# Performance work log

Measured on AMD Instinct MI355X. Metric: run time of the kernel, lower is better.

The kernel has to match this reference:

```python
import jax, jax.numpy as jnp
import numpy as np

HID = 128
HEADS = 4
CH = HID // HEADS          # 32
EDGE_DIM = 2 * HID         # H_update mode
GROUPS = 8
NEG_SLOPE = 0.2
EPS_GN = 1e-5
EPS_LN = 1e-5
N_NODES = 32768
N_EDGES = 524288


def setup_inputs() -> dict:
    key = jax.random.key(0)
    ks = jax.random.split(key, 32)
    N, E, C = N_NODES, N_EDGES, HID
    s = lambda fan: 1.0 / np.sqrt(fan)
    inp = dict(
        h_target=jax.random.normal(ks[0], (N, C), jnp.float32),
        h_source=jax.random.normal(ks[1], (N, C), jnp.float32),
        pos=jax.random.normal(ks[2], (N, 2), jnp.float32),
        t_emb=jax.random.normal(ks[3], (N, C), jnp.float32),
        edge_index=jax.random.randint(ks[4], (2, E), 0, N, jnp.int32),
        # AdaGN params
        gn_gamma=jnp.ones((C,), jnp.float32),
        gn_beta=jnp.zeros((C,), jnp.float32),
        fc_W=jax.random.normal(ks[5], (C, 2 * C), jnp.float32) * s(C),
        fc_b=jnp.zeros((2 * C,), jnp.float32),
        # GATv2 params
        Wl=jax.random.normal(ks[6], (C, HEADS * CH), jnp.float32) * s(C),
        bl=jnp.zeros((HEADS * CH,), jnp.float32),
        Wr=jax.random.normal(ks[7], (C, HEADS * CH), jnp.float32) * s(C),
        br=jnp.zeros((HEADS * CH,), jnp.float32),
        We=jax.random.normal(ks[8], (EDGE_DIM, HEADS * CH), jnp.float32) * s(EDGE_DIM),
        att=jax.random.normal(ks[9], (HEADS, CH), jnp.float32) * s(CH),
        gat_bias=jnp.zeros((HEADS * CH,), jnp.float32),
        # post GAT linear
        Wpost=jax.random.normal(ks[10], (C, C), jnp.float32) * s(C),
        bpost=jnp.zeros((C,), jnp.float32),
        # update MLP: LayerNorm -> Linear -> GELU -> Linear
        ln_g=jnp.ones((C,), jnp.float32),
        ln_b=jnp.zeros((C,), jnp.float32),
        W1=jax.random.normal(ks[11], (C, C), jnp.float32) * s(C),
        b1=jnp.zeros((C,), jnp.float32),
        W2=jax.random.normal(ks[12], (C, C), jnp.float32) * s(C),
        b2=jnp.zeros((C,), jnp.float32),
    )
    return inp


def _adagn(x, cond, gn_gamma, gn_beta, fc_W, fc_b):
    N, C = x.shape
    xg = x.reshape(N, GROUPS, C // GROUPS)
    mu = xg.mean(-1, keepdims=True)
    var = xg.var(-1, keepdims=True)
    normed = ((xg - mu) * jax.lax.rsqrt(var + EPS_GN)).reshape(N, C)
    normed = normed * gn_gamma + gn_beta
    style = cond @ fc_W + fc_b
    gamma, beta = jnp.split(style, 2, axis=-1)
    return normed * (1.0 + gamma) + beta


def reference(h_target, h_source, pos, t_emb, edge_index,
              gn_gamma, gn_beta, fc_W, fc_b,
              Wl, bl, Wr, br, We, att, gat_bias,
              Wpost, bpost, ln_g, ln_b, W1, b1, W2, b2):
    N, C = h_source.shape
    src, dst = edge_index[0], edge_index[1]

    h_src_mod = _adagn(h_source, t_emb, gn_gamma, gn_beta, fc_W, fc_b)

    # physics edge features (H_update mode)
    d_vec = pos[src] - pos[dst]                       # [E,2]
    dx, dy = d_vec[:, 0:1], d_vec[:, 1:2]
    dist_sq = jnp.maximum((d_vec ** 2).sum(-1, keepdims=True), 1e-8)
    grad_mag = (h_src_mod[src] - h_src_mod[dst]) / dist_sq   # [E,C]
    edge_attr = jnp.concatenate([grad_mag * (-dy), grad_mag * dx], axis=-1)  # [E,2C]

    # GATv2Conv (eval mode, no dropout)
    xl = (h_src_mod @ Wl + bl).reshape(N, HEADS, CH)  # source transform
    xr = (h_src_mod @ Wr + br).reshape(N, HEADS, CH)  # target transform
    e = (edge_attr @ We).reshape(-1, HEADS, CH)
    z = jax.nn.leaky_relu(xl[src] + xr[dst] + e, NEG_SLOPE)   # [E,H,Ch]
    logit = jnp.einsum('ehc,hc->eh', z, att)                  # [E,H]
    m = jax.ops.segment_max(logit, dst, num_segments=N)       # [N,H]
    m = jnp.where(jnp.isfinite(m), m, 0.0)
    ex = jnp.exp(logit - m[dst])
    denom = jax.ops.segment_sum(ex, dst, num_segments=N)      # [N,H]
    alpha = ex / (denom[dst] + 1e-16)                         # [E,H]
    msg = xl[src] * alpha[..., None]                          # [E,H,Ch]
    aggr = jax.ops.segment_sum(msg, dst, num_segments=N).reshape(N, HEADS * CH)
    aggr = aggr + gat_bias

    aggr = aggr @ Wpost + bpost

    # update MLP with residual
    mu = aggr.mean(-1, keepdims=True)
    var = aggr.var(-1, keepdims=True)
    ln = (aggr - mu) * jax.lax.rsqrt(var + EPS_LN) * ln_g + ln_b
    h = jax.nn.gelu(ln @ W1 + b1, approximate=False) @ W2 + b2
    return h_target + h
```

## Files before the change

### kernel.cpp

```cpp
#include <hip/hip_runtime.h>
#include <hip/hip_bf16.h>
#include <math.h>

#define HID 128

typedef __bf16 bf16x8 __attribute__((ext_vector_type(8)));
typedef float f32x4 __attribute__((ext_vector_type(4)));
typedef float nf4 __attribute__((ext_vector_type(4)));
union BF8 { uint4 u; bf16x8 v; unsigned short s[8]; };
struct U3 { unsigned x, y, z; };

__device__ __forceinline__ unsigned short f2bf(float x) {
  unsigned u = __float_as_uint(x);
  unsigned r = u + 0x7FFFu + ((u >> 16) & 1u);
  return (unsigned short)(r >> 16);
}
__device__ __forceinline__ float bf2f(unsigned short h) {
  return __uint_as_float(((unsigned)h) << 16);
}
__device__ __forceinline__ void ld2bf(const unsigned short* p, float& x, float& y) {
  unsigned v = *(const unsigned*)p;
  x = __uint_as_float((v & 0xFFFFu) << 16);
  y = __uint_as_float(v & 0xFFFF0000u);
}
__device__ __forceinline__ float2 unpk(unsigned w) {
  return make_float2(__uint_as_float(w << 16), __uint_as_float(w & 0xFFFF0000u));
}
__device__ __forceinline__ float2 pk_add2(float2 a, float2 b) {
  return make_float2(a.x + b.x, a.y + b.y);
}
__device__ __forceinline__ float2 pk_sub2(float2 a, float2 b) {
  return make_float2(a.x - b.x, a.y - b.y);
}
__device__ __forceinline__ float2 pk_fma2(float2 a, float2 b, float2 c) {
  return make_float2(fmaf(a.x, b.x, c.x), fmaf(a.y, b.y, c.y));
}
__device__ __forceinline__ float2 pk_max2(float2 a, float2 b) {
  return make_float2(fmaxf(a.x, b.x), fmaxf(a.y, b.y));
}
__device__ __forceinline__ float2 pk_muls2(float2 a, float b) {
  return make_float2(a.x * b, a.y * b);
}

__global__ __launch_bounds__(256) void k1_prep_zero(
    const float* __restrict__ fc_W, const float* __restrict__ Wl,
    const float* __restrict__ Wr, const float* __restrict__ We,
    const float* __restrict__ Wpost, const float* __restrict__ W1,
    const float* __restrict__ W2, const float* __restrict__ bl,
    const float* __restrict__ br, const float* __restrict__ gat_bias,
    const float* __restrict__ bpost,
    unsigned short* __restrict__ fcTh, unsigned short* __restrict__ fcTl,
    unsigned short* __restrict__ WnTh, unsigned short* __restrict__ WnTl,
    unsigned short* __restrict__ WpT, unsigned short* __restrict__ W1T,
    unsigned short* __restrict__ W2T,
    float* __restrict__ bxy, float* __restrict__ bpost2,
    int* __restrict__ count) {
  int bid = blockIdx.x;
  if (bid >= 578) {
    int i = (bid - 578) * 256 + threadIdx.x;
    ((int4*)count)[i] = make_int4(0, 0, 0, 0);
    return;
  }
  int gid = bid * 256 + threadIdx.x;
  if (gid < 32768) {
    int n = gid >> 7, k = gid & 127;
    float x = fc_W[k * 256 + n];
    unsigned short h = f2bf(x);
    fcTh[n * 128 + k] = h;
    fcTl[n * 128 + k] = f2bf(x - bf2f(h));
  } else if (gid < 98304) {
    int i = gid - 32768; int n = i >> 7, k = i & 127;
    float x;
    if (n < 128)      x = Wl[k * 128 + n];
    else if (n < 256) x = Wr[k * 128 + (n - 128)];
    else if (n < 384) x = We[k * 128 + (n - 256)];
    else              x = We[(128 + k) * 128 + (n - 384)];
    unsigned short h = f2bf(x);
    WnTh[n * 128 + k] = h;
    if (n >= 256) WnTl[(n - 256) * 128 + k] = f2bf(x - bf2f(h));
  } else if (gid < 147456) {
    int i = gid - 98304; int which = i >> 14; int j = i & 16383;
    int n = j >> 7, k = j & 127;
    const float* W = (which == 0) ? Wpost : (which == 1) ? W1 : W2;
    unsigned short* T = (which == 0) ? WpT : (which == 1) ? W1T : W2T;
    T[n * 128 + k] = f2bf(W[k * 128 + n]);
  } else if (gid < 147712) {
    int j = gid - 147456;
    bxy[j] = (j < 128) ? bl[j] : br[j - 128];
  } else if (gid < 147840) {
    int t = gid - 147712;
    float s = bpost[t];
    for (int k = 0; k < 128; ++k) s += gat_bias[k] * Wpost[k * 128 + t];
    bpost2[t] = s;
  }
}

__global__ __launch_bounds__(256) void k2_style_hist(
    const float* __restrict__ A, const unsigned short* __restrict__ WTh,
    const unsigned short* __restrict__ WTl, const float* __restrict__ bias,
    float* __restrict__ C,
    const int* __restrict__ edst, int* __restrict__ count, int E) {
  if (blockIdx.x >= 512) {
    int e = (blockIdx.x - 512) * 256 + threadIdx.x;
    if (e < E) atomicAdd(&count[edst[e]], 1);
    return;
  }
  int tid = threadIdx.x;
  int wave = tid >> 6, lane = tid & 63;
  int m = lane & 15, q = lane >> 4;
  int r0 = blockIdx.x * 64 + wave * 16;
  const float* arow = A + (size_t)(r0 + m) * 128 + q * 8;
  BF8 Ah[4], Al[4];
#pragma unroll
  for (int kc = 0; kc < 4; ++kc) {
    float4 x0 = *(const float4*)(arow + kc * 32);
    float4 x1 = *(const float4*)(arow + kc * 32 + 4);
    float xs[8] = {x0.x, x0.y, x0.z, x0.w, x1.x, x1.y, x1.z, x1.w};
#pragma unroll
    for (int j = 0; j < 8; ++j) {
      unsigned short h = f2bf(xs[j]);
      Ah[kc].s[j] = h;
      Al[kc].s[j] = f2bf(xs[j] - bf2f(h));
    }
  }
  for (int nt = 0; nt < 16; ++nt) {
    const unsigned short* wr  = WTh + (size_t)(nt * 16 + m) * 128 + q * 8;
    const unsigned short* wrl = WTl + (size_t)(nt * 16 + m) * 128 + q * 8;
    f32x4 acc = {0.f, 0.f, 0.f, 0.f};
#pragma unroll
    for (int kc = 0; kc < 4; ++kc) {
      BF8 bh, blo;
      bh.u  = *(const uint4*)(wr + kc * 32);
      blo.u = *(const uint4*)(wrl + kc * 32);
      acc = __builtin_amdgcn_mfma_f32_16x16x32_bf16(Ah[kc].v, bh.v, acc, 0, 0, 0);
      acc = __builtin_amdgcn_mfma_f32_16x16x32_bf16(Al[kc].v, bh.v, acc, 0, 0, 0);
      acc = __builtin_amdgcn_mfma_f32_16x16x32_bf16(Ah[kc].v, blo.v, acc, 0, 0, 0);
    }
    int n = nt * 16 + m;
    float bv = bias[n];
#pragma unroll
    for (int i = 0; i < 4; ++i) {
      int row = r0 + q * 4 + i;
      C[(size_t)row * 256 + n] = acc[i] + bv;
    }
  }
}

__global__ __launch_bounds__(256) void k3_node_scan(
    const float* __restrict__ h_source, const float* __restrict__ style,
    const float* __restrict__ gn_gamma, const float* __restrict__ gn_beta,
    const unsigned short* __restrict__ WnTh, const unsigned short* __restrict__ WnTl,
    const float* __restrict__ bxy,
    unsigned short* __restrict__ packed, unsigned short* __restrict__ xrArr,
    const int* __restrict__ count, int* __restrict__ rowptr,
    int* __restrict__ cursor, int N, int E) {
  if (blockIdx.x == 256) {
    __shared__ int wtot[4];
    int t = threadIdx.x, lane = t & 63, wv = t >> 6;
    const int4* c4 = (const int4*)count;
    int base = t * 32;
    int s = 0;
    for (int i = 0; i < 32; ++i) {
      int4 c = c4[base + i];
      s += c.x + c.y + c.z + c.w;
    }
    int incl = s;
#pragma unroll
    for (int off = 1; off < 64; off <<= 1) {
      int v = __shfl_up(incl, off);
      if (lane >= off) incl += v;
    }
    if (lane == 63) wtot[wv] = incl;
    __syncthreads();
    if (t == 0) {
      int a0 = wtot[0], a1 = wtot[1], a2 = wtot[2];
      wtot[0] = 0; wtot[1] = a0; wtot[2] = a0 + a1; wtot[3] = a0 + a1 + a2;
    }
    __syncthreads();
    int run = wtot[wv] + incl - s;
    for (int i = 0; i < 32; ++i) {
      int4 c = c4[base + i];
      int4 r;
      r.x = run; run += c.x;
      r.y = run; run += c.y;
      r.z = run; run += c.z;
      r.w = run; run += c.w;
      ((int4*)rowptr)[base + i] = r;
      ((int4*)cursor)[base + i] = r;
    }
    if (t == 255) rowptr[N] = E;
    return;
  }
  int tid = threadIdx.x, wave = tid >> 6, lane = tid & 63;
  int m = lane & 15, q = lane >> 4;
  int r0 = blockIdx.x * 128 + wave * 32;
  BF8 Ah[2][4], Al[2][4];
#pragma unroll
  for (int set = 0; set < 2; ++set) {
    int r = r0 + set * 16 + m;
    const float* hrow = h_source + (size_t)r * 128;
    const float* srow = style + (size_t)r * 256;
#pragma unroll
    for (int kc = 0; kc < 4; ++kc) {
      int ch = q * 8 + kc * 32;
      float4 x0 = *(const float4*)(hrow + ch);
      float4 x1 = *(const float4*)(hrow + ch + 4);
      float xs[8] = {x0.x, x0.y, x0.z, x0.w, x1.x, x1.y, x1.z, x1.w};
      float s8 = 0.f, q8 = 0.f;
#pragma unroll
      for (int j = 0; j < 8; ++j) { s8 += xs[j]; q8 += xs[j] * xs[j]; }
      float s16 = s8 + __shfl_xor(s8, 16);
      float q16 = q8 + __shfl_xor(q8, 16);
      float mu = s16 * (1.0f / 16.0f);
      float var = q16 * (1.0f / 16.0f) - mu * mu;
      float rv = rsqrtf(var + 1e-5f);
      float4 g0 = *(const float4*)(gn_gamma + ch);
      float4 g1 = *(const float4*)(gn_gamma + ch + 4);
      float4 be0 = *(const float4*)(gn_beta + ch);
      float4 be1 = *(const float4*)(gn_beta + ch + 4);
      float4 sg0 = *(const float4*)(srow + ch);
      float4 sg1 = *(const float4*)(srow + ch + 4);
      float4 sb0 = *(const float4*)(srow + 128 + ch);
      float4 sb1 = *(const float4*)(srow + 128 + ch + 4);
      float gg[8] = {g0.x, g0.y, g0.z, g0.w, g1.x, g1.y, g1.z, g1.w};
      float bb[8] = {be0.x, be0.y, be0.z, be0.w, be1.x, be1.y, be1.z, be1.w};
      float sg[8] = {sg0.x, sg0.y, sg0.z, sg0.w, sg1.x, sg1.y, sg1.z, sg1.w};
      float sb[8] = {sb0.x, sb0.y, sb0.z, sb0.w, sb1.x, sb1.y, sb1.z, sb1.w};
#pragma unroll
      for (int j = 0; j < 8; ++j) {
        float v = ((xs[j] - mu) * rv * gg[j] + bb[j]) * (1.0f + sg[j]) + sb[j];
        unsigned short h = f2bf(v);
        Ah[set][kc].s[j] = h;
        Al[set][kc].s[j] = f2bf(v - bf2f(h));
      }
    }
  }
  for (int nt = 0; nt < 32; ++nt) {
    f32x4 acc0 = {0.f, 0.f, 0.f, 0.f};
    f32x4 acc1 = {0.f, 0.f, 0.f, 0.f};
    const unsigned short* wr = WnTh + (size_t)(nt * 16 + m) * 128 + q * 8;
    if (nt < 16) {
#pragma unroll
      for (int kc = 0; kc < 4; ++kc) {
        BF8 bh; bh.u = *(const uint4*)(wr + kc * 32);
        acc0 = __builtin_amdgcn_mfma_f32_16x16x32_bf16(Ah[0][kc].v, bh.v, acc0, 0, 0, 0);
        acc1 = __builtin_amdgcn_mfma_f32_16x16x32_bf16(Ah[1][kc].v, bh.v, acc1, 0, 0, 0);
      }
    } else {
      const unsigned short* wl = WnTl + (size_t)((nt - 16) * 16 + m) * 128 + q * 8;
#pragma unroll
      for (int kc = 0; kc < 4; ++kc) {
        BF8 bh, blo;
        bh.u  = *(const uint4*)(wr + kc * 32);
        blo.u = *(const uint4*)(wl + kc * 32);
        acc0 = __builtin_amdgcn_mfma_f32_16x16x32_bf16(Ah[0][kc].v, bh.v, acc0, 0, 0, 0);
        acc0 = __builtin_amdgcn_mfma_f32_16x16x32_bf16(Al[0][kc].v, bh.v, acc0, 0, 0, 0);
        acc0 = __builtin_amdgcn_mfma_f32_16x16x32_bf16(Ah[0][kc].v, blo.v, acc0, 0, 0, 0);
        acc1 = __builtin_amdgcn_mfma_f32_16x16x32_bf16(Ah[1][kc].v, bh.v, acc1, 0, 0, 0);
        acc1 = __builtin_amdgcn_mfma_f32_16x16x32_bf16(Al[1][kc].v, bh.v, acc1, 0, 0, 0);
        acc1 = __builtin_amdgcn_mfma_f32_16x16x32_bf16(Ah[1][kc].v, blo.v, acc1, 0, 0, 0);
      }
    }
    int n = nt * 16 + m;
    float bv = (nt < 16) ? bxy[n] : 0.0f;
#pragma unroll
    for (int set = 0; set < 2; ++set) {
      f32x4 a = set ? acc1 : acc0;
#pragma unroll
      for (int i = 0; i < 4; ++i) {
        int row = r0 + set * 16 + q * 4 + i;
        unsigned short h = f2bf(a[i] + bv);
        size_t pb = (size_t)row * 384;
        if (nt < 8)       packed[pb + (n >> 1) * 6 + (n & 1)] = h;
        else if (nt < 16) xrArr[(size_t)row * 128 + (n - 128)] = h;
        else if (nt < 24) { int c = n - 256; packed[pb + (c >> 1) * 6 + 2 + (c & 1)] = h; }
        else              { int c = n - 384; packed[pb + (c >> 1) * 6 + 4 + (c & 1)] = h; }
      }
    }
  }
}

__global__ __launch_bounds__(256) void k_scatter(const int* __restrict__ esrc,
                                                 const int* __restrict__ edst,
                                                 const float* __restrict__ pos,
                                                 int* __restrict__ cursor,
                                                 nf4* __restrict__ meta, int E) {
  int e = blockIdx.x * 256 + threadIdx.x;
  if (e >= E) return;
  int src = esrc[e], dst = edst[e];
  int p = atomicAdd(&cursor[dst], 1);
  float2 ps = *(const float2*)(pos + 2 * src);
  float2 pd = *(const float2*)(pos + 2 * dst);
  float dx = ps.x - pd.x, dy = ps.y - pd.y;
  float d2 = fmaxf(dx * dx + dy * dy, 1e-8f);
  nf4 v = {__int_as_float(src), -dy / d2, dx / d2, 0.0f};
  meta[p] = v;
}

__device__ __forceinline__ void edge_step(nf4 mt, const U3* __restrict__ packed3,
                                          int lane, float2 xr, float2 Ad, float2 Bd,
                                          float a0, float a1,
                                          float& m, float& l, float2& s) {
  int si = __float_as_int(mt.x);
  U3 w = packed3[(size_t)si * 64 + lane];
  float2 xl = unpk(w.x);
  float2 A  = unpk(w.y);
  float2 B  = unpk(w.z);
  float2 z = pk_add2(xl, xr);
  z = pk_fma2(make_float2(mt.y, mt.y), pk_sub2(A, Ad), z);
  z = pk_fma2(make_float2(mt.z, mt.z), pk_sub2(B, Bd), z);
  float2 zl = pk_max2(z, pk_muls2(z, 0.2f));
  float p = fmaf(a0, zl.x, a1 * zl.y);
#pragma unroll
  for (int mm = 8; mm >= 1; mm >>= 1) p += __shfl_xor(p, mm);
  if (p <= m) {
    float ex = __expf(p - m);
    l += ex;
    s = pk_fma2(make_float2(ex, ex), xl, s);
  } else {
    float sc = __expf(m - p);
    l = fmaf(l, sc, 1.0f);
    s = pk_fma2(make_float2(sc, sc), s, xl);
    m = p;
  }
}

__global__ __launch_bounds__(256) void k_edge(const int* __restrict__ rowptr,
                                              const nf4* __restrict__ meta,
                                              const unsigned short* __restrict__ packed,
                                              const unsigned short* __restrict__ xrArr,
                                              const float* __restrict__ att,
                                              unsigned* __restrict__ aggr16, int N) {
  int tid = threadIdx.x;
  int d = blockIdx.x * 4 + (tid >> 6);
  if (d >= N) return;
  int lane = tid & 63;
  int c0 = lane * 2;
  float2 av = *(const float2*)(att + c0);
  const U3* packed3 = (const U3*)packed;
  float2 xr, Ad, Bd;
  ld2bf(xrArr + (size_t)d * 128 + c0, xr.x, xr.y);
  {
    U3 wd = packed3[(size_t)d * 64 + lane];
    Ad = unpk(wd.y);
    Bd = unpk(wd.z);
  }
  int beg = rowptr[d], end = rowptr[d + 1];
  float m1 = -INFINITY, l1 = 0.f; float2 s1 = make_float2(0.f, 0.f);
  float m2 = -INFINITY, l2 = 0.f; float2 s2 = make_float2(0.f, 0.f);
  int j = beg;
  if (j + 1 < end) {
    nf4 mt0 = meta[j], mt1 = meta[j + 1];
    for (; j + 3 < end; j += 2) {
      nf4 nx0 = meta[j + 2], nx1 = meta[j + 3];
      edge_step(mt0, packed3, lane, xr, Ad, Bd, av.x, av.y, m1, l1, s1);
      edge_step(mt1, packed3, lane, xr, Ad, Bd, av.x, av.y, m2, l2, s2);
      mt0 = nx0; mt1 = nx1;
    }
    edge_step(mt0, packed3, lane, xr, Ad, Bd, av.x, av.y, m1, l1, s1);
    edge_step(mt1, packed3, lane, xr, Ad, Bd, av.x, av.y, m2, l2, s2);
    j += 2;
  }
  if (j < end) {
    nf4 mt = meta[j];
    edge_step(mt, packed3, lane, xr, Ad, Bd, av.x, av.y, m1, l1, s1);
  }
  float nm = fmaxf(m1, m2);
  float sc1 = (m1 == nm) ? 1.0f : __expf(m1 - nm);
  float sc2 = (m2 == nm) ? 1.0f : __expf(m2 - nm);
  float l = fmaf(l1, sc1, l2 * sc2);
  float o0 = fmaf(s1.x, sc1, s2.x * sc2);
  float o1 = fmaf(s1.y, sc1, s2.y * sc2);
  float inv = 1.0f / (l + 1e-16f);
  aggr16[(size_t)d * 64 + lane] = (unsigned)f2bf(o0 * inv) | ((unsigned)f2bf(o1 * inv) << 16);
}

__global__ __launch_bounds__(256) void k_mlp(const unsigned short* __restrict__ aggr16,
                                             const unsigned short* __restrict__ WpT,
                                             const unsigned short* __restrict__ W1T,
                                             const unsigned short* __restrict__ W2T,
                                             const float* __restrict__ bpost2,
                                             const float* __restrict__ b1,
                                             const float* __restrict__ b2,
                                             const float* __restrict__ ln_g,
                                             const float* __restrict__ ln_b,
                                             const float* __restrict__ h_target,
                                             float* __restrict__ out) {
  __shared__ unsigned short Tb[64 * 136];
  __shared__ unsigned short Ub[64 * 136];
  int tid = threadIdx.x, wave = tid >> 6, lane = tid & 63;
  int m = lane & 15, q = lane >> 4;
  int r0 = blockIdx.x * 64 + wave * 16;
  int rb0 = wave * 16;
  BF8 Af[4];
  {
    const unsigned short* arow = aggr16 + (size_t)(r0 + m) * 128 + q * 8;
#pragma unroll
    for (int kc = 0; kc < 4; ++kc) Af[kc].u = *(const uint4*)(arow + kc * 32);
  }
  f32x4 acc[8];
#pragma unroll
  for (int t = 0; t < 8; ++t) {
    const unsigned short* wr = WpT + (size_t)(t * 16 + m) * 128 + q * 8;
    f32x4 a = {0.f, 0.f, 0.f, 0.f};
#pragma unroll
    for (int kc = 0; kc < 4; ++kc) {
      BF8 bh; bh.u = *(const uint4*)(wr + kc * 32);
      a = __builtin_amdgcn_mfma_f32_16x16x32_bf16(Af[kc].v, bh.v, a, 0, 0, 0);
    }
    acc[t] = a;
  }
  float sum[4] = {0, 0, 0, 0}, sq[4] = {0, 0, 0, 0};
#pragma unroll
  for (int t = 0; t < 8; ++t) {
    float bv = bpost2[t * 16 + m];
#pragma unroll
    for (int i = 0; i < 4; ++i) {
      float v = acc[t][i] + bv;
      acc[t][i] = v;
      sum[i] += v;
      sq[i] += v * v;
    }
  }
#pragma unroll
  for (int i = 0; i < 4; ++i) {
#pragma unroll
    for (int w = 1; w <= 8; w <<= 1) {
      sum[i] += __shfl_xor(sum[i], w);
      sq[i] += __shfl_xor(sq[i], w);
    }
  }
  float mu[4], rv[4];
#pragma unroll
  for (int i = 0; i < 4; ++i) {
    mu[i] = sum[i] * (1.0f / 128.0f);
    float var = sq[i] * (1.0f / 128.0f) - mu[i] * mu[i];
    rv[i] = rsqrtf(var + 1e-5f);
  }
#pragma unroll
  for (int t = 0; t < 8; ++t) {
    int n = t * 16 + m;
    float g = ln_g[n], b = ln_b[n];
#pragma unroll
    for (int i = 0; i < 4; ++i) {
      float v = (acc[t][i] - mu[i]) * rv[i] * g + b;
      Tb[(rb0 + q * 4 + i) * 136 + n] = f2bf(v);
    }
  }
  __syncthreads();
  BF8 Bf[4];
  {
    const unsigned short* tp = Tb + (rb0 + m) * 136 + q * 8;
#pragma unroll
    for (int kc = 0; kc < 4; ++kc) Bf[kc].u = *(const uint4*)(tp + kc * 32);
  }
#pragma unroll
  for (int t = 0; t < 8; ++t) {
    const unsigned short* wr = W1T + (size_t)(t * 16 + m) * 128 + q * 8;
    f32x4 a = {0.f, 0.f, 0.f, 0.f};
#pragma unroll
    for (int kc = 0; kc < 4; ++kc) {
      BF8 bh; bh.u = *(const uint4*)(wr + kc * 32);
      a = __builtin_amdgcn_mfma_f32_16x16x32_bf16(Bf[kc].v, bh.v, a, 0, 0, 0);
    }
    acc[t] = a;
  }
#pragma unroll
  for (int t = 0; t < 8; ++t) {
    int n = t * 16 + m;
    float bv = b1[n];
#pragma unroll
    for (int i = 0; i < 4; ++i) {
      float v = acc[t][i] + bv;
      v = 0.5f * v * (1.0f + erff(v * 0.70710678118654752f));
      Ub[(rb0 + q * 4 + i) * 136 + n] = f2bf(v);
    }
  }
  __syncthreads();
  BF8 Cf[4];
  {
    const unsigned short* up = Ub + (rb0 + m) * 136 + q * 8;
#pragma unroll
    for (int kc = 0; kc < 4; ++kc) Cf[kc].u = *(const uint4*)(up + kc * 32);
  }
#pragma unroll
  for (int t = 0; t < 8; ++t) {
    const unsigned short* wr = W2T + (size_t)(t * 16 + m) * 128 + q * 8;
    f32x4 a = {0.f, 0.f, 0.f, 0.f};
#pragma unroll
    for (int kc = 0; kc < 4; ++kc) {
      BF8 bh; bh.u = *(const uint4*)(wr + kc * 32);
      a = __builtin_amdgcn_mfma_f32_16x16x32_bf16(Cf[kc].v, bh.v, a, 0, 0, 0);
    }
    int n = t * 16 + m;
    float bv = b2[n];
#pragma unroll
    for (int i = 0; i < 4; ++i) {
      size_t off = (size_t)(r0 + q * 4 + i) * 128 + n;
      out[off] = a[i] + bv + h_target[off];
    }
  }
}

extern "C" void kernel_launch(void* const* d_in, const int* in_sizes, int n_in,
                              void* d_out, int out_size, void* d_ws, size_t ws_size,
                              hipStream_t stream) {
  const float* h_target = (const float*)d_in[0];
  const float* h_source = (const float*)d_in[1];
  const float* pos      = (const float*)d_in[2];
  const float* t_emb    = (const float*)d_in[3];
  const int*   eidx     = (const int*)d_in[4];
  const float* gn_gamma = (const float*)d_in[5];
  const float* gn_beta  = (const float*)d_in[6];
  const float* fc_W     = (const float*)d_in[7];
  const float* fc_b     = (const float*)d_in[8];
  const float* Wl       = (const float*)d_in[9];
  const float* bl       = (const float*)d_in[10];
  const float* Wr       = (const float*)d_in[11];
  const float* br       = (const float*)d_in[12];
  const float* We       = (const float*)d_in[13];
  const float* att      = (const float*)d_in[14];
  const float* gat_bias = (const float*)d_in[15];
  const float* Wpost    = (const float*)d_in[16];
  const float* bpost    = (const float*)d_in[17];
  const float* ln_g     = (const float*)d_in[18];
  const float* ln_b     = (const float*)d_in[19];
  const float* W1       = (const float*)d_in[20];
  const float* b1       = (const float*)d_in[21];
  const float* W2       = (const float*)d_in[22];
  const float* b2       = (const float*)d_in[23];

  const int N = in_sizes[0] / HID;
  const int E = in_sizes[4] / 2;
  const int* esrc = eidx;
  const int* edst = eidx + E;

  float* ws = (float*)d_ws;
  const size_t MF = 1024 * 1024;
  float* style  = ws;
  unsigned* aggr16 = (unsigned*)ws;
  unsigned short* packed = (unsigned short*)(ws + 8 * MF);
  unsigned short* xrArr  = (unsigned short*)(ws + 14 * MF);
  nf4*   meta   = (nf4*)(ws + 16 * MF);
  int*   rowptr = (int*)(ws + 18 * MF);
  int*   count  = rowptr + 32832;
  int*   cursor = count + 32832;
  unsigned short* wgt = (unsigned short*)(ws + 18 * MF + 131072);
  unsigned short* fcTh = wgt;
  unsigned short* fcTl = wgt + 32768;
  unsigned short* WnTh = wgt + 65536;
  unsigned short* WnTl = wgt + 131072;
  unsigned short* WpT  = wgt + 163840;
  unsigned short* W1T  = wgt + 180224;
  unsigned short* W2T  = wgt + 196608;
  float* bxy    = (float*)(wgt + 212992);
  float* bpost2 = bxy + 256;
  const size_t needed = (size_t)(18 * MF + 131072 + 106496 + 512) * 4;
  if (ws_size < needed) return;

  dim3 blk(256);
  const int histB = (E + 255) / 256;

  k1_prep_zero<<<610, blk, 0, stream>>>(
      fc_W, Wl, Wr, We, Wpost, W1, W2, bl, br, gat_bias, bpost,
      fcTh, fcTl, WnTh, WnTl, WpT, W1T, W2T, bxy, bpost2, count);
  k2_style_hist<<<512 + histB, blk, 0, stream>>>(t_emb, fcTh, fcTl, fc_b, style,
                                                 edst, count, E);
  k3_node_scan<<<257, blk, 0, stream>>>(h_source, style, gn_gamma, gn_beta, WnTh, WnTl,
                                        bxy, packed, xrArr, count, rowptr, cursor, N, E);
  k_scatter<<<histB, blk, 0, stream>>>(esrc, edst, pos, cursor, meta, E);
  k_edge<<<(N + 3) / 4, blk, 0, stream>>>(rowptr, meta, packed, xrArr, att, aggr16, N);
  k_mlp<<<N / 64, blk, 0, stream>>>((const unsigned short*)aggr16, WpT, W1T, W2T, bpost2,
                                    b1, b2, ln_g, ln_b, h_target, (float*)d_out);
}
```

Baseline: 364.1 us.

## Stage MFMA outputs through swizzled LDS for coalesced global stores

The three GEMM kernels (style projection, node transform, final MLP) now write their MFMA accumulator fragments into per-wave shared memory, using XOR swizzles or padding, and then store full rows to global memory with wide coalesced writes. Before, each lane wrote scattered scalar floats or bf16 values. The node kernel now processes its two row sets one after another so the LDS tile fits, and the xr array is written and read as packed 32-bit words. The cost is large LDS allocations (64KB in k2 and k3), which limit occupancy, and the node kernel loses the weight-load reuse it had from interleaving the two sets.

```diff
diff --git a/kernel.cpp b/kernel.cpp
--- a/kernel.cpp
+++ b/kernel.cpp
@@ -17,11 +17,6 @@
 }
 __device__ __forceinline__ float bf2f(unsigned short h) {
   return __uint_as_float(((unsigned)h) << 16);
-}
-__device__ __forceinline__ void ld2bf(const unsigned short* p, float& x, float& y) {
-  unsigned v = *(const unsigned*)p;
-  x = __uint_as_float((v & 0xFFFFu) << 16);
-  y = __uint_as_float(v & 0xFFFF0000u);
 }
 __device__ __forceinline__ float2 unpk(unsigned w) {
   return make_float2(__uint_as_float(w << 16), __uint_as_float(w & 0xFFFF0000u));
@@ -100,6 +95,7 @@
     const unsigned short* __restrict__ WTl, const float* __restrict__ bias,
     float* __restrict__ C,
     const int* __restrict__ edst, int* __restrict__ count, int E) {
+  __shared__ float Lsf[16384];
   if (blockIdx.x >= 512) {
     int e = (blockIdx.x - 512) * 256 + threadIdx.x;
     if (e < E) atomicAdd(&count[edst[e]], 1);
@@ -109,6 +105,7 @@
   int wave = tid >> 6, lane = tid & 63;
   int m = lane & 15, q = lane >> 4;
   int r0 = blockIdx.x * 64 + wave * 16;
+  int wbase = wave * 4096;
   const float* arow = A + (size_t)(r0 + m) * 128 + q * 8;
   BF8 Ah[4], Al[4];
 #pragma unroll
@@ -140,9 +137,14 @@
     float bv = bias[n];
 #pragma unroll
     for (int i = 0; i < 4; ++i) {
-      int row = r0 + q * 4 + i;
-      C[(size_t)row * 256 + n] = acc[i] + bv;
-    }
+      int rl = q * 4 + i;
+      Lsf[wbase + rl * 256 + (n ^ (4 * (rl & 7)))] = acc[i] + bv;
+    }
+  }
+  for (int r = 0; r < 16; ++r) {
+    int cc = (4 * lane) ^ (4 * (r & 7));
+    float4 v = *(const float4*)&Lsf[wbase + r * 256 + cc];
+    *(float4*)&C[(size_t)(r0 + r) * 256 + 4 * lane] = v;
   }
 }
 
@@ -151,11 +153,12 @@
     const float* __restrict__ gn_gamma, const float* __restrict__ gn_beta,
     const unsigned short* __restrict__ WnTh, const unsigned short* __restrict__ WnTl,
     const float* __restrict__ bxy,
-    unsigned short* __restrict__ packed, unsigned short* __restrict__ xrArr,
+    unsigned short* __restrict__ packed, unsigned* __restrict__ xrArr32,
     const int* __restrict__ count, int* __restrict__ rowptr,
     int* __restrict__ cursor, int N, int E) {
+  __shared__ int poolI[16384];
   if (blockIdx.x == 256) {
-    __shared__ int wtot[4];
+    int* wtot = poolI;
     int t = threadIdx.x, lane = t & 63, wv = t >> 6;
     const int4* c4 = (const int4*)count;
     int base = t * 32;
@@ -172,12 +175,12 @@
     }
     if (lane == 63) wtot[wv] = incl;
     __syncthreads();
-    if (t == 0) {
-      int a0 = wtot[0], a1 = wtot[1], a2 = wtot[2];
-      wtot[0] = 0; wtot[1] = a0; wtot[2] = a0 + a1; wtot[3] = a0 + a1 + a2;
-    }
-    __syncthreads();
-    int run = wtot[wv] + incl - s;
+    int run0 = 0;
+    for (int w = 0; w < 4; ++w) {
+      if (w == wv) break;
+      run0 += wtot[w];
+    }
+    int run = run0 + incl - s;
     for (int i = 0; i < 32; ++i) {
       int4 c = c4[base + i];
       int4 r;
@@ -191,9 +194,11 @@
     if (t == 255) rowptr[N] = E;
     return;
   }
+  unsigned short* Ls = (unsigned short*)poolI;
   int tid = threadIdx.x, wave = tid >> 6, lane = tid & 63;
   int m = lane & 15, q = lane >> 4;
   int r0 = blockIdx.x * 128 + wave * 32;
+  int wbase = wave * 8192;
   BF8 Ah[2][4], Al[2][4];
 #pragma unroll
   for (int set = 0; set < 2; ++set) {
@@ -235,47 +240,48 @@
       }
     }
   }
-  for (int nt = 0; nt < 32; ++nt) {
-    f32x4 acc0 = {0.f, 0.f, 0.f, 0.f};
-    f32x4 acc1 = {0.f, 0.f, 0.f, 0.f};
-    const unsigned short* wr = WnTh + (size_t)(nt * 16 + m) * 128 + q * 8;
-    if (nt < 16) {
-#pragma unroll
-      for (int kc = 0; kc < 4; ++kc) {
-        BF8 bh; bh.u = *(const uint4*)(wr + kc * 32);
-        acc0 = __builtin_amdgcn_mfma_f32_16x16x32_bf16(Ah[0][kc].v, bh.v, acc0, 0, 0, 0);
-        acc1 = __builtin_amdgcn_mfma_f32_16x16x32_bf16(Ah[1][kc].v, bh.v, acc1, 0, 0, 0);
+  U3* packed3 = (U3*)packed;
+  for (int set = 0; set < 2; ++set) {
+    for (int nt = 0; nt < 32; ++nt) {
+      f32x4 acc = {0.f, 0.f, 0.f, 0.f};
+      const unsigned short* wr = WnTh + (size_t)(nt * 16 + m) * 128 + q * 8;
+      if (nt < 16) {
+#pragma unroll
+        for (int kc = 0; kc < 4; ++kc) {
+          BF8 bh; bh.u = *(const uint4*)(wr + kc * 32);
+          acc = __builtin_amdgcn_mfma_f32_16x16x32_bf16(Ah[set][kc].v, bh.v, acc, 0, 0, 0);
+        }
+      } else {
+        const unsigned short* wl = WnTl + (size_t)((nt - 16) * 16 + m) * 128 + q * 8;
+#pragma unroll
+        for (int kc = 0; kc < 4; ++kc) {
+          BF8 bh, blo;
+          bh.u  = *(const uint4*)(wr + kc * 32);
+          blo.u = *(const uint4*)(wl + kc * 32);
+          acc = __builtin_amdgcn_mfma_f32_16x16x32_bf16(Ah[set][kc].v, bh.v, acc, 0, 0, 0);
+          acc = __builtin_amdgcn_mfma_f32_16x16x32_bf16(Al[set][kc].v, bh.v, acc, 0, 0, 0);
+          acc = __builtin_amdgcn_mfma_f32_16x16x32_bf16(Ah[set][kc].v, blo.v, acc, 0, 0, 0);
+        }
       }
-    } else {
-      const unsigned short* wl = WnTl + (size_t)((nt - 16) * 16 + m) * 128 + q * 8;
-#pragma unroll
-      for (int kc = 0; kc < 4; ++kc) {
-        BF8 bh, blo;
-        bh.u  = *(const uint4*)(wr + kc * 32);
-        blo.u = *(const uint4*)(wl + kc * 32);
-        acc0 = __builtin_amdgcn_mfma_f32_16x16x32_bf16(Ah[0][kc].v, bh.v, acc0, 0, 0, 0);
-        acc0 = __builtin_amdgcn_mfma_f32_16x16x32_bf16(Al[0][kc].v, bh.v, acc0, 0, 0, 0);
-        acc0 = __builtin_amdgcn_mfma_f32_16x16x32_bf16(Ah[0][kc].v, blo.v, acc0, 0, 0, 0);
-        acc1 = __builtin_amdgcn_mfma_f32_16x16x32_bf16(Ah[1][kc].v, bh.v, acc1, 0, 0, 0);
-        acc1 = __builtin_amdgcn_mfma_f32_16x16x32_bf16(Al[1][kc].v, bh.v, acc1, 0, 0, 0);
-        acc1 = __builtin_amdgcn_mfma_f32_16x16x32_bf16(Ah[1][kc].v, blo.v, acc1, 0, 0, 0);
+      int n = nt * 16 + m;
+      float bv = (nt < 16) ? bxy[n] : 0.0f;
+#pragma unroll
+      for (int i = 0; i < 4; ++i) {
+        int rl = q * 4 + i;
+        Ls[wbase + rl * 512 + (n ^ (8 * (rl & 7)))] = f2bf(acc[i] + bv);
       }
     }
-    int n = nt * 16 + m;
-    float bv = (nt < 16) ? bxy[n] : 0.0f;
-#pragma unroll
-    for (int set = 0; set < 2; ++set) {
-      f32x4 a = set ? acc1 : acc0;
-#pragma unroll
-      for (int i = 0; i < 4; ++i) {
-        int row = r0 + set * 16 + q * 4 + i;
-        unsigned short h = f2bf(a[i] + bv);
-        size_t pb = (size_t)row * 384;
-        if (nt < 8)       packed[pb + (n >> 1) * 6 + (n & 1)] = h;
-        else if (nt < 16) xrArr[(size_t)row * 128 + (n - 128)] = h;
-        else if (nt < 24) { int c = n - 256; packed[pb + (c >> 1) * 6 + 2 + (c & 1)] = h; }
-        else              { int c = n - 384; packed[pb + (c >> 1) * 6 + 4 + (c & 1)] = h; }
-      }
+    for (int r = 0; r < 16; ++r) {
+      int p = lane ^ (4 * (r & 7));
+      const unsigned* Lrow = (const unsigned*)(Ls + wbase + r * 512);
+      unsigned xl = Lrow[p];
+      unsigned xr = Lrow[64 + p];
+      unsigned Aa = Lrow[128 + p];
+      unsigned Bb = Lrow[192 + p];
+      int row = r0 + set * 16 + r;
+      U3 w3; w3.x = xl; w3.y = Aa; w3.z = Bb;
+      packed3[(size_t)row * 64 + lane] = w3;
+      xrArr32[(size_t)row * 64 + lane] = xr;
     }
   }
 }
@@ -328,7 +334,7 @@
 __global__ __launch_bounds__(256) void k_edge(const int* __restrict__ rowptr,
                                               const nf4* __restrict__ meta,
                                               const unsigned short* __restrict__ packed,
-                                              const unsigned short* __restrict__ xrArr,
+                                              const unsigned* __restrict__ xrArr32,
                                               const float* __restrict__ att,
                                               unsigned* __restrict__ aggr16, int N) {
   int tid = threadIdx.x;
@@ -339,7 +345,7 @@
   float2 av = *(const float2*)(att + c0);
   const U3* packed3 = (const U3*)packed;
   float2 xr, Ad, Bd;
-  ld2bf(xrArr + (size_t)d * 128 + c0, xr.x, xr.y);
+  xr = unpk(xrArr32[(size_t)d * 64 + lane]);
   {
     U3 wd = packed3[(size_t)d * 64 + lane];
     Ad = unpk(wd.y);
@@ -386,8 +392,9 @@
                                              const float* __restrict__ ln_b,
                                              const float* __restrict__ h_target,
                                              float* __restrict__ out) {
-  __shared__ unsigned short Tb[64 * 136];
-  __shared__ unsigned short Ub[64 * 136];
+  __shared__ int pool[8704];
+  unsigned short* Tb = (unsigned short*)pool;
+  unsigned short* Ub = Tb + 8704;
   int tid = threadIdx.x, wave = tid >> 6, lane = tid & 63;
   int m = lane & 15, q = lane >> 4;
   int r0 = blockIdx.x * 64 + wave * 16;
@@ -483,6 +490,9 @@
 #pragma unroll
     for (int kc = 0; kc < 4; ++kc) Cf[kc].u = *(const uint4*)(up + kc * 32);
   }
+  __syncthreads();
+  float* Fb = (float*)pool;
+  int fbase = wave * 2112;
 #pragma unroll
   for (int t = 0; t < 8; ++t) {
     const unsigned short* wr = W2T + (size_t)(t * 16 + m) * 128 + q * 8;
@@ -495,10 +505,14 @@
     int n = t * 16 + m;
     float bv = b2[n];
 #pragma unroll
-    for (int i = 0; i < 4; ++i) {
-      size_t off = (size_t)(r0 + q * 4 + i) * 128 + n;
-      out[off] = a[i] + bv + h_target[off];
-    }
+    for (int i = 0; i < 4; ++i)
+      Fb[fbase + (q * 4 + i) * 132 + n] = a[i] + bv;
+  }
+  for (int r = 0; r < 16; ++r) {
+    float2 v = *(const float2*)&Fb[fbase + r * 132 + 2 * lane];
+    size_t off = (size_t)(r0 + r) * 128 + 2 * lane;
+    float2 h = *(const float2*)&h_target[off];
+    *(float2*)&out[off] = make_float2(v.x + h.x, v.y + h.y);
   }
 }
 
@@ -540,7 +554,7 @@
   float* style  = ws;
   unsigned* aggr16 = (unsigned*)ws;
   unsigned short* packed = (unsigned short*)(ws + 8 * MF);
-  unsigned short* xrArr  = (unsigned short*)(ws + 14 * MF);
+  unsigned* xrArr32 = (unsigned*)(ws + 14 * MF);
   nf4*   meta   = (nf4*)(ws + 16 * MF);
   int*   rowptr = (int*)(ws + 18 * MF);
   int*   count  = rowptr + 32832;
@@ -567,9 +581,9 @@
   k2_style_hist<<<512 + histB, blk, 0, stream>>>(t_emb, fcTh, fcTl, fc_b, style,
                                                  edst, count, E);
   k3_node_scan<<<257, blk, 0, stream>>>(h_source, style, gn_gamma, gn_beta, WnTh, WnTl,
-                                        bxy, packed, xrArr, count, rowptr, cursor, N, E);
+                                        bxy, packed, xrArr32, count, rowptr, cursor, N, E);
   k_scatter<<<histB, blk, 0, stream>>>(esrc, edst, pos, cursor, meta, E);
-  k_edge<<<(N + 3) / 4, blk, 0, stream>>>(rowptr, meta, packed, xrArr, att, aggr16, N);
+  k_edge<<<(N + 3) / 4, blk, 0, stream>>>(rowptr, meta, packed, xrArr32, att, aggr16, N);
   k_mlp<<<N / 64, blk, 0, stream>>>((const unsigned short*)aggr16, WpT, W1T, W2T, bpost2,
                                     b1, b2, ln_g, ln_b, h_target, (float*)d_out);
 }
```

After: 384.1 us. +5.5%, slower.
